# Optimization experiments

Hardware: AMD Instinct MI355X
Metric: run time of the kernel (lower is better)

Reference implementation:

```python
import jax, jax.numpy as jnp
from jax import lax
import numpy as np

ALPHA = 0.1
GAMMA = 0.001
PIXELS = 50
BIG = 1e8  # finite stand-in for +inf so softmin grads stay clean


def setup_inputs() -> dict:
    key = jax.random.key(0)
    k1, k2, k3 = jax.random.split(key, 3)
    B, T, H, W = 64, 24, 256, 256
    pred = jax.random.normal(k1, (B, T, 1, H, W), dtype=jnp.float32)
    true = jax.random.normal(k2, (B, T, 1, H, W), dtype=jnp.float32)
    static_ch = jax.random.uniform(k3, (B, 1, 1, H, W), dtype=jnp.float32)
    return {"pred": pred, "true": true, "static_ch": static_ch}


def _softmin3(a, b, c, gamma):
    x = jnp.stack([a, b, c])
    return -gamma * jax.nn.logsumexp(-x / gamma, axis=0)


def _soft_dtw_value(D, gamma):
    # D: (N, N) local cost matrix; classic soft-DTW DP, R[N, N] returned.
    N = D.shape[0]
    r0 = jnp.full((N + 1,), BIG, dtype=D.dtype).at[0].set(0.0)  # row i=0

    def row_step(r_prev, d_row):
        def col_step(left, inp):
            d, diag, up = inp
            r = d + _softmin3(diag, up, left, gamma)
            return r, r
        _, r_vals = lax.scan(col_step, jnp.asarray(BIG, D.dtype),
                             (d_row, r_prev[:-1], r_prev[1:]))
        r_cur = jnp.concatenate([jnp.full((1,), BIG, D.dtype), r_vals])
        return r_cur, None

    r_last, _ = lax.scan(row_step, r0, D)
    return r_last[-1]


def _sample_top_pixels(true, pred, mask, pixels):
    # Faithful to sample_top_pixels_modified, including the raw .view(-1, T, 1)
    # reshape of the (B, T, 1, pixels) gathered tensors.
    B, T = true.shape[0], true.shape[1]
    HW = true.shape[3] * true.shape[4]
    mask_flat = mask.reshape(B, -1)                       # (B, HW)
    _, top_idx = lax.top_k(mask_flat, pixels)             # (B, pixels)
    idx = jnp.broadcast_to(top_idx[:, None, None, :], (B, T, 1, pixels))
    tf = true.reshape(B, T, 1, HW)
    pf = pred.reshape(B, T, 1, HW)
    gt = jnp.take_along_axis(tf, idx, axis=-1)            # (B, T, 1, pixels)
    gp = jnp.take_along_axis(pf, idx, axis=-1)
    return gt.reshape(-1, T, 1), gp.reshape(-1, T, 1)     # (B*pixels, T, 1)


def _dilate(outputs, targets, alpha, gamma):
    # outputs = sampled_pred, targets = sampled_true; shapes (BS, N, 1)
    BS, N = outputs.shape[0], outputs.shape[1]
    t = targets[:, :, 0]
    p = outputs[:, :, 0]
    # pairwise_distances(targets_k, outputs_k) = squared diffs, clamped >= 0
    D = jnp.maximum((t[:, :, None] - p[:, None, :]) ** 2, 0.0)  # (BS, N, N)

    def dtw_sum(Dm):
        return jnp.sum(jax.vmap(lambda Dk: _soft_dtw_value(Dk, gamma))(Dm))

    loss_shape = dtw_sum(D) / BS
    # PathDTWBatch = d(soft-dtw)/dD per sample, averaged over batch
    path = jnp.mean(jax.grad(dtw_sum)(D), axis=0)         # (N, N)
    rng = jnp.arange(1, N + 1, dtype=D.dtype)             # torch.range(1, N)
    Omega = (rng[:, None] - rng[None, :]) ** 2            # (N, N)
    loss_temporal = jnp.sum(path * Omega) / (N * N)
    return alpha * loss_shape + (1.0 - alpha) * loss_temporal


def reference(pred, true, static_ch):
    sampled_true, sampled_pred = _sample_top_pixels(true, pred, static_ch, PIXELS)
    return _dilate(sampled_pred, sampled_true, ALPHA, GAMMA)
```

## Files before the change

### kernel.cpp

```cpp
#include <hip/hip_runtime.h>
#include <math.h>

#define BATCH 64
#define TT 24
#define HW 65536
#define PIX 50
#define NN 24
#define GAMMA_F 0.001f
#define INVG 1000.0f
#define BIGF 100000000.0f
#define PARTS 4
#define PSIZE (HW / PARTS)
#define CAPL 512
#define NBLK 1600
#define NCAND (PARTS * PIX)

__device__ __forceinline__ unsigned ordered_key(float f) {
    unsigned u = __float_as_uint(f);
    return (u & 0x80000000u) ? ~u : (u | 0x80000000u);
}

__global__ __launch_bounds__(1024) void topk_local_kernel(
        const float* __restrict__ mask, unsigned long long* __restrict__ cands) {
    __shared__ unsigned keys[PSIZE];
    __shared__ unsigned long long wred[16];
    __shared__ unsigned long long bc;
    __shared__ unsigned ck[CAPL];
    __shared__ unsigned ci[CAPL];
    __shared__ unsigned ncand;

    const int tid  = threadIdx.x;
    const int w    = tid >> 6;
    const int lane = tid & 63;
    const int b    = blockIdx.x >> 2;
    const int part = blockIdx.x & 3;
    if (tid == 0) ncand = 0;

    const float4* m4 = (const float4*)(mask + (size_t)b * HW + part * PSIZE);
    for (int c = tid; c < PSIZE / 4; c += 1024) {
        float4 v = m4[c];
        uint4 k;
        k.x = ordered_key(v.x);
        k.y = ordered_key(v.y);
        k.z = ordered_key(v.z);
        k.w = ordered_key(v.w);
        ((uint4*)keys)[c] = k;
    }
    __syncthreads();

    unsigned pref = 0, himask = 0;
    unsigned remaining = PIX;
    for (int d = 7; d >= 0; --d) {
        const int sh = 2 * d;
        unsigned long long acc = 0;
        for (int c = tid; c < PSIZE; c += 1024) {
            unsigned k16 = keys[c] >> 16;
            if ((k16 & himask) == pref) {
                unsigned q = (k16 >> sh) & 3u;
                acc += 1ull << (16 * q);
            }
        }
        #pragma unroll
        for (int off = 32; off > 0; off >>= 1) acc += __shfl_down(acc, off);
        if (lane == 0) wred[w] = acc;
        __syncthreads();
        if (tid == 0) {
            unsigned long long t = 0;
            #pragma unroll
            for (int i = 0; i < 16; ++i) t += wred[i];
            bc = t;
        }
        __syncthreads();
        const unsigned long long C = bc;
        unsigned S = 0, sel = 0;
        #pragma unroll
        for (int q = 3; q >= 0; --q) {
            unsigned c = (unsigned)((C >> (16 * q)) & 0xFFFFull);
            if (S + c >= remaining) { sel = (unsigned)q; remaining -= S; break; }
            S += c;
        }
        pref   |= sel << sh;
        himask |= 3u << sh;
    }
    const unsigned thresh = pref;

    for (int c = tid; c < PSIZE; c += 1024) {
        unsigned k = keys[c];
        if ((k >> 16) >= thresh) {
            unsigned pos = atomicAdd(&ncand, 1u);
            if (pos < CAPL) { ck[pos] = k; ci[pos] = (unsigned)(part * PSIZE + c); }
        }
    }
    __syncthreads();

    const int nc = (int)min(ncand, (unsigned)CAPL);
    for (int c = tid; c < nc; c += 1024) {
        unsigned long long me =
            ((unsigned long long)ck[c] << 32) | (unsigned long long)(~ci[c]);
        int rank = 0;
        for (int j = 0; j < nc; ++j) {
            unsigned long long o =
                ((unsigned long long)ck[j] << 32) | (unsigned long long)(~ci[j]);
            rank += (o > me);
        }
        if (rank < PIX) cands[(size_t)blockIdx.x * PIX + rank] = me;
    }
}

__global__ __launch_bounds__(256) void merge_kernel(
        const unsigned long long* __restrict__ cands, int* __restrict__ topIdx) {
    __shared__ unsigned long long cl[NCAND];
    const int b   = blockIdx.x;
    const int tid = threadIdx.x;
    for (int i = tid; i < NCAND; i += 256) cl[i] = cands[(size_t)b * NCAND + i];
    __syncthreads();
    if (tid < NCAND) {
        unsigned long long me = cl[tid];
        int rank = 0;
        for (int j = 0; j < NCAND; ++j) rank += (cl[j] > me);
        if (rank < PIX) topIdx[b * PIX + rank] = (int)(~(unsigned)(me & 0xFFFFFFFFull));
    }
}

__global__ __launch_bounds__(64, 2) void dtw_kernel(
        const float* __restrict__ pred, const float* __restrict__ truth,
        const int* __restrict__ topIdx, float2* __restrict__ parts) {
    __shared__ float Rr[64][27];
    __shared__ float P[64];

    const int lane = threadIdx.x;
    const int half = lane >> 5;
    const int r    = lane & 31;
    const bool rowAct = (r < NN);

    const int np  = 2 * blockIdx.x + half;
    const int b   = np / PIX;
    const int npb = np - b * PIX;

    float tv = 0.0f, pv = 0.0f;
    if (rowAct) {
        int f  = npb * NN + r;
        int t  = f / PIX;
        int pp = f - t * PIX;
        size_t a = (size_t)(b * TT + t) * HW + (size_t)topIdx[b * PIX + pp];
        tv = truth[a];
        pv = pred[a];
    }
    P[lane] = pv;

    float Rprev = BIGF, Rprev2 = BIGF;
    #pragma unroll
    for (int s = 2; s <= 2 * NN; ++s) {
        int j = s - 1 - r;
        bool act = rowAct && (j >= 1) && (j <= NN);
        float up   = __shfl_up(Rprev, 1);
        float diag = __shfl_up(Rprev2, 1);
        int jc = j - 1; jc = jc < 0 ? 0 : (jc > NN - 1 ? NN - 1 : jc);
        float pj = P[(half << 5) + jc];
        if (r == 0) { up = BIGF; diag = (s == 2) ? 0.0f : BIGF; }
        float mn = fminf(diag, fminf(up, Rprev));
        float z = __expf((mn - diag) * INVG) + __expf((mn - up) * INVG)
                + __expf((mn - Rprev) * INVG);
        float d = tv - pj;
        float Rnew = d * d + mn - GAMMA_F * __logf(z);
        if (act) {
            Rr[lane][j - 1] = Rnew;
            Rprev2 = Rprev;
            Rprev  = Rnew;
        }
    }
    float accS = 0.0f, accT = 0.0f;
    if (r == NN - 1) accS = Rprev;

    float Eprev = 0.0f, Eprev2 = 0.0f;
    if (r == NN - 1) Eprev = 1.0f;
    float tnext = __shfl_down(tv, 1);
    #pragma unroll
    for (int s = 2 * NN - 1; s >= 2; --s) {
        int j = s - 1 - r;
        bool act = rowAct && (j >= 1) && (j <= NN);
        float eUp   = __shfl_down(Eprev, 1);
        float eDiag = __shfl_down(Eprev2, 1);
        int jc  = j - 1; jc  = jc  < 0 ? 0 : (jc  > NN - 1 ? NN - 1 : jc);
        int jc2 = j;     jc2 = jc2 < 0 ? 0 : (jc2 > NN - 1 ? NN - 1 : jc2);
        int lup = (r < NN - 1) ? lane + 1 : lane;
        float rij    = Rr[lane][jc];
        float rRight = (j >= NN)                ? -INFINITY : Rr[lane][jc2];
        float rDown  = (r == NN - 1)            ? -INFINITY : Rr[lup][jc];
        float rDiag  = (r == NN - 1 || j >= NN) ? -INFINITY : Rr[lup][jc2];
        float pjm1 = P[(half << 5) + jc];
        float pj   = P[(half << 5) + jc2];
        float da = tnext - pjm1; da *= da;
        float db = tv - pj;      db *= db;
        float dc = tnext - pj;   dc *= dc;
        float aw = __expf((rDown  - rij - da) * INVG);
        float bw = __expf((rRight - rij - db) * INVG);
        float cw = __expf((rDiag  - rij - dc) * INVG);
        float Enew = aw * eUp + bw * Eprev + cw * eDiag;
        if (act) {
            float dd = (float)(r + 1 - j);
            accT += Enew * dd * dd;
            Eprev2 = Eprev;
            Eprev  = Enew;
        }
    }

    #pragma unroll
    for (int off = 32; off > 0; off >>= 1) {
        accS += __shfl_xor(accS, off);
        accT += __shfl_xor(accT, off);
    }
    if (lane == 0) parts[blockIdx.x] = make_float2(accS, accT);
}

__global__ void finalize_kernel(const float2* __restrict__ parts,
                                float* __restrict__ out) {
    __shared__ double sd[256];
    __shared__ double td[256];
    int tid = threadIdx.x;
    double s = 0.0, t = 0.0;
    for (int i = tid; i < NBLK; i += 256) {
        float2 v = parts[i];
        s += (double)v.x;
        t += (double)v.y;
    }
    sd[tid] = s; td[tid] = t;
    __syncthreads();
    for (int off = 128; off > 0; off >>= 1) {
        if (tid < off) { sd[tid] += sd[tid + off]; td[tid] += td[tid + off]; }
        __syncthreads();
    }
    if (tid == 0) {
        double loss_shape    = sd[0] / (double)(BATCH * PIX);
        double loss_temporal = td[0] / ((double)(BATCH * PIX) * (double)(NN * NN));
        out[0] = (float)(0.1 * loss_shape + 0.9 * loss_temporal);
    }
}

extern "C" void kernel_launch(void* const* d_in, const int* in_sizes, int n_in,
                              void* d_out, int out_size, void* d_ws, size_t ws_size,
                              hipStream_t stream) {
    const float* pred  = (const float*)d_in[0];
    const float* truth = (const float*)d_in[1];
    const float* mask  = (const float*)d_in[2];

    char* ws = (char*)d_ws;
    unsigned long long* cands = (unsigned long long*)ws;
    int*    topIdx = (int*)(ws + 102400);
    float2* parts  = (float2*)(ws + 102400 + 12800);

    topk_local_kernel<<<BATCH * PARTS, 1024, 0, stream>>>(mask, cands);
    merge_kernel<<<BATCH, 256, 0, stream>>>(cands, topIdx);
    dtw_kernel<<<NBLK, 64, 0, stream>>>(pred, truth, topIdx, parts);
    finalize_kernel<<<1, 256, 0, stream>>>(parts, (float*)d_out);
}
```

Baseline: 56.96 us.

## Use 4-bit radix digits and fuse first histogram pass into key load

The top-k threshold radix select now works on 4-bit digits in 4 passes instead of 2-bit digits in 8 passes. This halves the number of block-wide barriers and shared-memory scans. The first pass's histogram is computed while converting the float keys, which removes one full rescan. Counts are packed as 4-bit nibbles and widened into 16-bit fields every two iterations so they cannot overflow. Keys are read from shared memory as uint4, and the reduction now carries four 64-bit words per thread.

Result: faster. 51.26 us (-10.0%).

```diff
diff --git a/kernel.cpp b/kernel.cpp
--- a/kernel.cpp
+++ b/kernel.cpp
@@ -20,11 +20,21 @@
     return (u & 0x80000000u) ? ~u : (u | 0x80000000u);
 }
 
+__device__ __forceinline__ void expand_add(unsigned long long a4,
+                                           unsigned long long* a16) {
+    #pragma unroll
+    for (int f = 0; f < 4; ++f) {
+        unsigned long long x = (a4 >> (16 * f)) & 0xFFFFull;
+        a16[f] += (x & 0xFull) | ((x & 0xF0ull) << 12)
+                | ((x & 0xF00ull) << 24) | ((x & 0xF000ull) << 36);
+    }
+}
+
 __global__ __launch_bounds__(1024) void topk_local_kernel(
         const float* __restrict__ mask, unsigned long long* __restrict__ cands) {
     __shared__ unsigned keys[PSIZE];
-    __shared__ unsigned long long wred[16];
-    __shared__ unsigned long long bc;
+    __shared__ unsigned long long wred[16][4];
+    __shared__ unsigned long long sBC[4];
     __shared__ unsigned ck[CAPL];
     __shared__ unsigned ci[CAPL];
     __shared__ unsigned ncand;
@@ -36,59 +46,86 @@
     const int part = blockIdx.x & 3;
     if (tid == 0) ncand = 0;
 
+    unsigned long long a16[4] = {0, 0, 0, 0};
+
     const float4* m4 = (const float4*)(mask + (size_t)b * HW + part * PSIZE);
-    for (int c = tid; c < PSIZE / 4; c += 1024) {
-        float4 v = m4[c];
-        uint4 k;
-        k.x = ordered_key(v.x);
-        k.y = ordered_key(v.y);
-        k.z = ordered_key(v.z);
-        k.w = ordered_key(v.w);
-        ((uint4*)keys)[c] = k;
-    }
-    __syncthreads();
-
-    unsigned pref = 0, himask = 0;
-    unsigned remaining = PIX;
-    for (int d = 7; d >= 0; --d) {
-        const int sh = 2 * d;
-        unsigned long long acc = 0;
-        for (int c = tid; c < PSIZE; c += 1024) {
-            unsigned k16 = keys[c] >> 16;
-            if ((k16 & himask) == pref) {
-                unsigned q = (k16 >> sh) & 3u;
-                acc += 1ull << (16 * q);
+    {
+        unsigned long long a4 = 0;
+        #pragma unroll
+        for (int i = 0; i < 4; ++i) {
+            int c = tid + 1024 * i;
+            float4 v = m4[c];
+            uint4 k;
+            k.x = ordered_key(v.x); k.y = ordered_key(v.y);
+            k.z = ordered_key(v.z); k.w = ordered_key(v.w);
+            ((uint4*)keys)[c] = k;
+            a4 += 1ull << (4 * (k.x >> 28));
+            a4 += 1ull << (4 * (k.y >> 28));
+            a4 += 1ull << (4 * (k.z >> 28));
+            a4 += 1ull << (4 * (k.w >> 28));
+            if (i & 1) { expand_add(a4, a16); a4 = 0; }
+        }
+    }
+
+    unsigned pref = 0, himask = 0, remaining = PIX;
+    #pragma unroll
+    for (int d = 3; d >= 0; --d) {
+        const int sh = 4 * d;
+        if (d < 3) {
+            a16[0] = a16[1] = a16[2] = a16[3] = 0;
+            unsigned long long a4 = 0;
+            #pragma unroll
+            for (int i = 0; i < 4; ++i) {
+                uint4 k = ((const uint4*)keys)[tid + 1024 * i];
+                unsigned k16;
+                k16 = k.x >> 16; if ((k16 & himask) == pref) a4 += 1ull << (4 * ((k16 >> sh) & 0xFu));
+                k16 = k.y >> 16; if ((k16 & himask) == pref) a4 += 1ull << (4 * ((k16 >> sh) & 0xFu));
+                k16 = k.z >> 16; if ((k16 & himask) == pref) a4 += 1ull << (4 * ((k16 >> sh) & 0xFu));
+                k16 = k.w >> 16; if ((k16 & himask) == pref) a4 += 1ull << (4 * ((k16 >> sh) & 0xFu));
+                if (i & 1) { expand_add(a4, a16); a4 = 0; }
             }
         }
         #pragma unroll
-        for (int off = 32; off > 0; off >>= 1) acc += __shfl_down(acc, off);
-        if (lane == 0) wred[w] = acc;
+        for (int off = 32; off > 0; off >>= 1) {
+            a16[0] += __shfl_down(a16[0], off);
+            a16[1] += __shfl_down(a16[1], off);
+            a16[2] += __shfl_down(a16[2], off);
+            a16[3] += __shfl_down(a16[3], off);
+        }
+        if (lane == 0) {
+            wred[w][0] = a16[0]; wred[w][1] = a16[1];
+            wred[w][2] = a16[2]; wred[w][3] = a16[3];
+        }
         __syncthreads();
-        if (tid == 0) {
+        if (tid < 4) {
             unsigned long long t = 0;
             #pragma unroll
-            for (int i = 0; i < 16; ++i) t += wred[i];
-            bc = t;
+            for (int i = 0; i < 16; ++i) t += wred[i][tid];
+            sBC[tid] = t;
         }
         __syncthreads();
-        const unsigned long long C = bc;
         unsigned S = 0, sel = 0;
         #pragma unroll
-        for (int q = 3; q >= 0; --q) {
-            unsigned c = (unsigned)((C >> (16 * q)) & 0xFFFFull);
-            if (S + c >= remaining) { sel = (unsigned)q; remaining -= S; break; }
+        for (int q = 15; q >= 0; --q) {
+            unsigned c = (unsigned)((sBC[q >> 2] >> (16 * (q & 3))) & 0xFFFFull);
+            if (S + c >= remaining) { sel = (unsigned)q; break; }
             S += c;
         }
+        remaining -= S;
         pref   |= sel << sh;
-        himask |= 3u << sh;
+        himask |= 0xFu << sh;
     }
     const unsigned thresh = pref;
 
-    for (int c = tid; c < PSIZE; c += 1024) {
-        unsigned k = keys[c];
-        if ((k >> 16) >= thresh) {
-            unsigned pos = atomicAdd(&ncand, 1u);
-            if (pos < CAPL) { ck[pos] = k; ci[pos] = (unsigned)(part * PSIZE + c); }
+    for (int c = tid; c < PSIZE / 4; c += 1024) {
+        uint4 k = ((const uint4*)keys)[c];
+        unsigned kk[4] = {k.x, k.y, k.z, k.w};
+        #pragma unroll
+        for (int e = 0; e < 4; ++e) {
+            if ((kk[e] >> 16) >= thresh) {
+                unsigned pos = atomicAdd(&ncand, 1u);
+                if (pos < CAPL) { ck[pos] = kk[e]; ci[pos] = (unsigned)(part * PSIZE + 4 * c + e); }
+            }
         }
     }
     __syncthreads();
```
